# Kernel optimization log

Hardware: AMD Instinct MI355X
Metric: run time of the kernel (lower is better)

The kernel has to match this reference:

```python
import jax, jax.numpy as jnp
import numpy as np

EPS = 1e-12  # torch F.normalize eps


def setup_inputs() -> dict:
    key = jax.random.key(0)
    k1, k2, k3 = jax.random.split(key, 3)
    N, C, H, W = 64, 512, 30, 30
    K = 64
    x = jax.random.normal(k1, (N, C, H, W), dtype=jnp.float32)
    # 1x1 conv weight [K, C] (kernel spatial dims squeezed out)
    conv_w = jax.random.normal(k2, (K, C), dtype=jnp.float32) * 0.04
    centroids = jax.random.uniform(k3, (K, C), dtype=jnp.float32)
    return {"x": x, "conv_w": conv_w, "centroids": centroids}


def reference(x, conv_w, centroids):
    N, C, H, W = x.shape
    K = conv_w.shape[0]
    # descriptor-wise L2 normalize over channel dim (normalize_input=True)
    nrm = jnp.sqrt(jnp.sum(x * x, axis=1, keepdims=True))
    x = x / jnp.maximum(nrm, EPS)
    xf = x.reshape(N, C, H * W)                       # [N, C, P]
    # 1x1 conv == per-pixel matmul: [N, K, P]
    logits = jnp.einsum("kc,ncp->nkp", conv_w, xf)
    a = jax.nn.softmax(logits, axis=1)                # softmax over clusters
    # vlad[n,k,c] = sum_p a[n,k,p] * (xf[n,c,p] - centroids[k,c])
    #            = (a @ xf^T) - sum_p(a) * centroids   (GEMM decomposition)
    agg = jnp.einsum("nkp,ncp->nkc", a, xf)           # [N, K, C]
    vlad = agg - a.sum(axis=-1)[:, :, None] * centroids[None]
    return vlad
```

## Files before the change

kernel.cpp:

```cpp
#include <hip/hip_runtime.h>
#include <math.h>

#define N_DIM 64
#define C_DIM 512
#define K_DIM 64
#define P_DIM 900
#define P_PAD 928
#define PTILES 15
#define XS_STRIDE 1040

typedef __attribute__((ext_vector_type(8))) short short8;
typedef __attribute__((ext_vector_type(4))) float f32x4;

#define A2_ELEMS   ((size_t)N_DIM * K_DIM * P_PAD)

__device__ inline ushort f2bf(float f) {
  uint u = __builtin_bit_cast(uint, f);
  u += 0x7FFFu + ((u >> 16) & 1u);
  return (ushort)(u >> 16);
}

__global__ __launch_bounds__(256) void netvlad_assign(
    const float* __restrict__ x, const float* __restrict__ w,
    ushort* __restrict__ a2, float* __restrict__ asum_part)
{
  const int n = blockIdx.y, bpt = blockIdx.x, p0 = bpt * 64;
  const int tid = threadIdx.x, wave = tid >> 6, lane = tid & 63;
  const int l15 = lane & 15, lhi = lane >> 4;

  __shared__ char  xs[64 * XS_STRIDE];
  __shared__ float red[4][64];
  __shared__ float invn_s[64];
  __shared__ float wredm[4][4][16];
  __shared__ float wreds[4][4][16];

  const float* xb = x + (size_t)n * C_DIM * P_DIM;
  const int ps = tid & 63;
  const int cq = (tid >> 6) * 4;
  const int gp = p0 + ps;
  const bool pv = gp < P_DIM;
  float ssq = 0.f;
  for (int c0 = 0; c0 < C_DIM; c0 += 16) {
    int c = c0 + cq;
    float v0 = pv ? xb[(size_t)(c + 0) * P_DIM + gp] : 0.f;
    float v1 = pv ? xb[(size_t)(c + 1) * P_DIM + gp] : 0.f;
    float v2 = pv ? xb[(size_t)(c + 2) * P_DIM + gp] : 0.f;
    float v3 = pv ? xb[(size_t)(c + 3) * P_DIM + gp] : 0.f;
    ssq += v0 * v0 + v1 * v1 + v2 * v2 + v3 * v3;
    unsigned long long pk =
        (unsigned long long)f2bf(v0) | ((unsigned long long)f2bf(v1) << 16) |
        ((unsigned long long)f2bf(v2) << 32) | ((unsigned long long)f2bf(v3) << 48);
    *(unsigned long long*)(xs + (size_t)ps * XS_STRIDE + (size_t)c * 2) = pk;
  }
  red[wave][ps] = ssq;

  short8 wfrag[16];
  const float* wrow = w + (size_t)(wave * 16 + l15) * C_DIM + lhi * 8;
#pragma unroll
  for (int ks = 0; ks < 16; ++ks) {
    float4 f0 = *(const float4*)(wrow + ks * 32);
    float4 f1 = *(const float4*)(wrow + ks * 32 + 4);
    short8 t;
    t[0] = (short)f2bf(f0.x); t[1] = (short)f2bf(f0.y);
    t[2] = (short)f2bf(f0.z); t[3] = (short)f2bf(f0.w);
    t[4] = (short)f2bf(f1.x); t[5] = (short)f2bf(f1.y);
    t[6] = (short)f2bf(f1.z); t[7] = (short)f2bf(f1.w);
    wfrag[ks] = t;
  }
  __syncthreads();

  if (tid < 64) {
    float s = red[0][tid] + red[1][tid] + red[2][tid] + red[3][tid];
    invn_s[tid] = ((p0 + tid) < P_DIM) ? (1.0f / fmaxf(sqrtf(s), 1e-12f)) : 0.f;
  }

  f32x4 acc[4];
#pragma unroll
  for (int pt = 0; pt < 4; ++pt) acc[pt] = (f32x4){0.f, 0.f, 0.f, 0.f};
#pragma unroll
  for (int ks = 0; ks < 16; ++ks) {
#pragma unroll
    for (int pt = 0; pt < 4; ++pt) {
      short8 xfrag = *(const short8*)(xs + (size_t)(pt * 16 + l15) * XS_STRIDE
                                         + ks * 64 + lhi * 16);
      acc[pt] = __builtin_amdgcn_mfma_f32_16x16x32_bf16(wfrag[ks], xfrag, acc[pt], 0, 0, 0);
    }
  }
  __syncthreads();

  float lg[4][4], linv[4];
#pragma unroll
  for (int pt = 0; pt < 4; ++pt) {
    linv[pt] = invn_s[pt * 16 + l15];
    float m = -1e30f;
#pragma unroll
    for (int r = 0; r < 4; ++r) { lg[pt][r] = acc[pt][r] * linv[pt]; m = fmaxf(m, lg[pt][r]); }
    m = fmaxf(m, __shfl_xor(m, 16));
    m = fmaxf(m, __shfl_xor(m, 32));
    if (lhi == 0) wredm[wave][pt][l15] = m;
  }
  __syncthreads();
#pragma unroll
  for (int pt = 0; pt < 4; ++pt) {
    float m = fmaxf(fmaxf(wredm[0][pt][l15], wredm[1][pt][l15]),
                    fmaxf(wredm[2][pt][l15], wredm[3][pt][l15]));
    float s = 0.f;
#pragma unroll
    for (int r = 0; r < 4; ++r) { lg[pt][r] = __expf(lg[pt][r] - m); s += lg[pt][r]; }
    s += __shfl_xor(s, 16);
    s += __shfl_xor(s, 32);
    if (lhi == 0) wreds[wave][pt][l15] = s;
  }
  __syncthreads();

  ushort* a2b = a2 + (size_t)n * K_DIM * P_PAD;
  float asr[4] = {0.f, 0.f, 0.f, 0.f};
#pragma unroll
  for (int pt = 0; pt < 4; ++pt) {
    float stot = wreds[0][pt][l15] + wreds[1][pt][l15] +
                 wreds[2][pt][l15] + wreds[3][pt][l15];
    float rs = 1.0f / stot;
    int p = p0 + pt * 16 + l15;
    bool vv = p < P_DIM;
#pragma unroll
    for (int r = 0; r < 4; ++r) {
      float a = lg[pt][r] * rs;
      if (vv) asr[r] += a;
      if (p < P_PAD) {
        int k = wave * 16 + lhi * 4 + r;
        a2b[(size_t)k * P_PAD + p] = vv ? f2bf(a * linv[pt]) : (ushort)0;
      }
    }
  }
#pragma unroll
  for (int r = 0; r < 4; ++r) {
    float v = asr[r];
    v += __shfl_xor(v, 1); v += __shfl_xor(v, 2);
    v += __shfl_xor(v, 4); v += __shfl_xor(v, 8);
    if (l15 == 0) {
      int k = wave * 16 + lhi * 4 + r;
      asum_part[((size_t)n * K_DIM + k) * PTILES + bpt] = v;
    }
  }
}

__global__ __launch_bounds__(256) void netvlad_agg(
    const float* __restrict__ x, const ushort* __restrict__ a2,
    const float* __restrict__ asum_part, const float* __restrict__ cent,
    float* __restrict__ out)
{
  const int n = blockIdx.y, ct = blockIdx.x, c0 = ct * 64;
  const int tid = threadIdx.x, wave = tid >> 6, lane = tid & 63;
  const int l15 = lane & 15, lhi = lane >> 4;

  __shared__ float asum_s[64];
  if (tid < 64) {
    const float* ap = asum_part + ((size_t)n * K_DIM + tid) * PTILES;
    float s = 0.f;
#pragma unroll
    for (int j = 0; j < PTILES; ++j) s += ap[j];
    asum_s[tid] = s;
  }
  __syncthreads();

  f32x4 acc[4];
#pragma unroll
  for (int mt = 0; mt < 4; ++mt) acc[mt] = (f32x4){0.f, 0.f, 0.f, 0.f};

  const float*  xrow = x + (size_t)n * C_DIM * P_DIM
                         + (size_t)(c0 + wave * 16 + l15) * P_DIM;
  const ushort* ab   = a2 + (size_t)n * K_DIM * P_PAD;

  for (int ks = 0; ks < 29; ++ks) {
    int pb = ks * 32 + lhi * 8;
    short8 bfrag;
    if (pb + 8 <= P_DIM) {
      float4 f0 = *(const float4*)(xrow + pb);
      float4 f1 = *(const float4*)(xrow + pb + 4);
      bfrag[0] = (short)f2bf(f0.x); bfrag[1] = (short)f2bf(f0.y);
      bfrag[2] = (short)f2bf(f0.z); bfrag[3] = (short)f2bf(f0.w);
      bfrag[4] = (short)f2bf(f1.x); bfrag[5] = (short)f2bf(f1.y);
      bfrag[6] = (short)f2bf(f1.z); bfrag[7] = (short)f2bf(f1.w);
    } else {
#pragma unroll
      for (int j = 0; j < 8; ++j)
        bfrag[j] = (pb + j < P_DIM) ? (short)f2bf(xrow[pb + j]) : (short)0;
    }
#pragma unroll
    for (int mt = 0; mt < 4; ++mt) {
      short8 afrag = *(const short8*)(ab + (size_t)(mt * 16 + l15) * P_PAD
                                         + ks * 32 + lhi * 8);
      acc[mt] = __builtin_amdgcn_mfma_f32_16x16x32_bf16(afrag, bfrag, acc[mt], 0, 0, 0);
    }
  }

  const int c = c0 + wave * 16 + l15;
#pragma unroll
  for (int mt = 0; mt < 4; ++mt) {
#pragma unroll
    for (int r = 0; r < 4; ++r) {
      int k = mt * 16 + lhi * 4 + r;
      out[((size_t)n * K_DIM + k) * C_DIM + c] =
          acc[mt][r] - asum_s[k] * cent[(size_t)k * C_DIM + c];
    }
  }
}

extern "C" void kernel_launch(void* const* d_in, const int* in_sizes, int n_in,
                              void* d_out, int out_size, void* d_ws, size_t ws_size,
                              hipStream_t stream) {
  const float* x    = (const float*)d_in[0];
  const float* w    = (const float*)d_in[1];
  const float* cent = (const float*)d_in[2];
  float* out = (float*)d_out;

  ushort* a2        = (ushort*)d_ws;
  float*  asum_part = (float*)((char*)d_ws + A2_ELEMS * sizeof(ushort));

  netvlad_assign<<<dim3(PTILES, N_DIM), 256, 0, stream>>>(x, w, a2, asum_part);
  netvlad_agg   <<<dim3(8, N_DIM),      256, 0, stream>>>(x, a2, asum_part, cent, out);
}
```

Measured before the change: 93.09 us.

## Load x fragments directly from global in assign kernel, dropping LDS staging

Removes the shared-memory staging of the bf16 x tile and the block-wide norm reduction in the assignment kernel. Each wave now reads its own x fragments straight from global memory, computes partial squared norms, and reduces them with cross-lane shuffles. The aim is to free the large LDS allocation and two barriers, which should allow higher occupancy. The cost is that all four waves re-read the same x tile, and the loads are strided gathers of 64-byte pieces, which adds L2 traffic.

```diff
diff --git a/kernel.cpp b/kernel.cpp
--- a/kernel.cpp
+++ b/kernel.cpp
@@ -7,7 +7,6 @@
 #define P_DIM 900
 #define P_PAD 928
 #define PTILES 15
-#define XS_STRIDE 1040
 
 typedef __attribute__((ext_vector_type(8))) short short8;
 typedef __attribute__((ext_vector_type(4))) float f32x4;
@@ -28,31 +27,8 @@
   const int tid = threadIdx.x, wave = tid >> 6, lane = tid & 63;
   const int l15 = lane & 15, lhi = lane >> 4;
 
-  __shared__ char  xs[64 * XS_STRIDE];
-  __shared__ float red[4][64];
-  __shared__ float invn_s[64];
   __shared__ float wredm[4][4][16];
   __shared__ float wreds[4][4][16];
-
-  const float* xb = x + (size_t)n * C_DIM * P_DIM;
-  const int ps = tid & 63;
-  const int cq = (tid >> 6) * 4;
-  const int gp = p0 + ps;
-  const bool pv = gp < P_DIM;
-  float ssq = 0.f;
-  for (int c0 = 0; c0 < C_DIM; c0 += 16) {
-    int c = c0 + cq;
-    float v0 = pv ? xb[(size_t)(c + 0) * P_DIM + gp] : 0.f;
-    float v1 = pv ? xb[(size_t)(c + 1) * P_DIM + gp] : 0.f;
-    float v2 = pv ? xb[(size_t)(c + 2) * P_DIM + gp] : 0.f;
-    float v3 = pv ? xb[(size_t)(c + 3) * P_DIM + gp] : 0.f;
-    ssq += v0 * v0 + v1 * v1 + v2 * v2 + v3 * v3;
-    unsigned long long pk =
-        (unsigned long long)f2bf(v0) | ((unsigned long long)f2bf(v1) << 16) |
-        ((unsigned long long)f2bf(v2) << 32) | ((unsigned long long)f2bf(v3) << 48);
-    *(unsigned long long*)(xs + (size_t)ps * XS_STRIDE + (size_t)c * 2) = pk;
-  }
-  red[wave][ps] = ssq;
 
   short8 wfrag[16];
   const float* wrow = w + (size_t)(wave * 16 + l15) * C_DIM + lhi * 8;
@@ -67,31 +43,52 @@
     t[6] = (short)f2bf(f1.z); t[7] = (short)f2bf(f1.w);
     wfrag[ks] = t;
   }
-  __syncthreads();
-
-  if (tid < 64) {
-    float s = red[0][tid] + red[1][tid] + red[2][tid] + red[3][tid];
-    invn_s[tid] = ((p0 + tid) < P_DIM) ? (1.0f / fmaxf(sqrtf(s), 1e-12f)) : 0.f;
+
+  const float* xb = x + (size_t)n * C_DIM * P_DIM;
+  const float* xcol[4];
+#pragma unroll
+  for (int pt = 0; pt < 4; ++pt) {
+    int pp = p0 + pt * 16 + l15;
+    xcol[pt] = xb + (pp < P_DIM ? pp : (P_DIM - 1));
   }
 
   f32x4 acc[4];
 #pragma unroll
   for (int pt = 0; pt < 4; ++pt) acc[pt] = (f32x4){0.f, 0.f, 0.f, 0.f};
-#pragma unroll
+  float ssqp[4] = {0.f, 0.f, 0.f, 0.f};
+
   for (int ks = 0; ks < 16; ++ks) {
+    const size_t coff = (size_t)(ks * 32 + lhi * 8) * P_DIM;
 #pragma unroll
     for (int pt = 0; pt < 4; ++pt) {
-      short8 xfrag = *(const short8*)(xs + (size_t)(pt * 16 + l15) * XS_STRIDE
-                                         + ks * 64 + lhi * 16);
-      acc[pt] = __builtin_amdgcn_mfma_f32_16x16x32_bf16(wfrag[ks], xfrag, acc[pt], 0, 0, 0);
-    }
-  }
-  __syncthreads();
-
-  float lg[4][4], linv[4];
-#pragma unroll
-  for (int pt = 0; pt < 4; ++pt) {
-    linv[pt] = invn_s[pt * 16 + l15];
+      const float* src = xcol[pt] + coff;
+      float v0 = src[0 * P_DIM], v1 = src[1 * P_DIM];
+      float v2 = src[2 * P_DIM], v3 = src[3 * P_DIM];
+      float v4 = src[4 * P_DIM], v5 = src[5 * P_DIM];
+      float v6 = src[6 * P_DIM], v7 = src[7 * P_DIM];
+      ssqp[pt] += v0 * v0 + v1 * v1 + v2 * v2 + v3 * v3
+                + v4 * v4 + v5 * v5 + v6 * v6 + v7 * v7;
+      short8 xf;
+      xf[0] = (short)f2bf(v0); xf[1] = (short)f2bf(v1);
+      xf[2] = (short)f2bf(v2); xf[3] = (short)f2bf(v3);
+      xf[4] = (short)f2bf(v4); xf[5] = (short)f2bf(v5);
+      xf[6] = (short)f2bf(v6); xf[7] = (short)f2bf(v7);
+      acc[pt] = __builtin_amdgcn_mfma_f32_16x16x32_bf16(wfrag[ks], xf, acc[pt], 0, 0, 0);
+    }
+  }
+
+  float linv[4];
+#pragma unroll
+  for (int pt = 0; pt < 4; ++pt) {
+    float s = ssqp[pt];
+    s += __shfl_xor(s, 16);
+    s += __shfl_xor(s, 32);
+    linv[pt] = 1.0f / fmaxf(sqrtf(s), 1e-12f);
+  }
+
+  float lg[4][4];
+#pragma unroll
+  for (int pt = 0; pt < 4; ++pt) {
     float m = -1e30f;
 #pragma unroll
     for (int r = 0; r < 4; ++r) { lg[pt][r] = acc[pt][r] * linv[pt]; m = fmaxf(m, lg[pt][r]); }
```

After: 100.4 us. 7.8% more time.
